# Optimization experiments

Measured on AMD Instinct MI355X. Metric: run time of the kernel, lower is better.

## Reference

```python
import jax, jax.numpy as jnp
import numpy as np

K, MU, SIGMA = 8, 0.0, 0.1
M, N, D_DIM, T = 512, 1024, 512, 4096


def setup_inputs() -> dict:
    key = jax.random.key(0)
    ks, ke, ka, kd, kl1, kl2 = jax.random.split(key, 6)
    S = jax.random.normal(ks, (N, T), dtype=jnp.float32)
    E = jax.random.normal(ke, (M, T), dtype=jnp.float32)  # raw noise; scaled by sigma/mu in reference
    A = jax.random.uniform(ka, (M, N), dtype=jnp.float32)  # torch.rand init
    Dm = jax.random.normal(kd, (N, D_DIM), dtype=jnp.float32) / jnp.sqrt(N)  # stands in for DCT-transformed randn
    c = jnp.ones((1,), dtype=jnp.float32)
    l1 = 0.1 * jnp.abs(jax.random.normal(kl1, (1,), dtype=jnp.float32)) + 0.05
    l2 = jax.random.normal(kl2, (1,), dtype=jnp.float32)
    # LISTA params per layer; all K layers get the same closed-form init in the original
    U1 = jnp.eye(D_DIM, dtype=jnp.float32) - (1.0 / c[0]) * (Dm.T @ A.T @ A @ Dm)  # [d,d]
    V1 = (1.0 / c[0]) * (Dm.T @ A.T)  # [d,m]
    U = jnp.broadcast_to(U1, (K, D_DIM, D_DIM)).copy()
    V = jnp.broadcast_to(V1, (K, D_DIM, M)).copy()
    H0 = jnp.zeros((D_DIM, T), dtype=jnp.float32)
    return {"S": S, "E": E, "A": A, "D": Dm, "U": U, "V": V, "l1": l1, "l2": l2, "c": c, "H0": H0}


def reference(S, E, A, D, U, V, l1, l2, c, H0):
    # X = A @ S + noise (E ~ randn, scaled as in torch forward)
    X = A @ S + (E * SIGMA + MU)  # [m,T]
    # Self-attention on H0 (the original loop always feeds self.H, the zero buffer,
    # into every layer -- H is never chained). Attention map = softmax((D@H0)^T (D@H0)).
    G = D @ H0                                   # [n,T]
    attn = jax.nn.softmax(G.T @ G, axis=-1)      # [T,T]
    Z = l2[0] * (H0 @ attn)                      # [d,T]
    # All K LISTA updates share the same (H0-derived) Z and X -> batch over layers.
    mat = jnp.einsum('kde,et->kdt', U, Z) + jnp.einsum('kdm,mt->kdt', V, X)  # [K,d,T]
    thres = l1[0] / c[0]
    H_all = jnp.sign(mat) * jnp.maximum(jnp.zeros((), mat.dtype), jnp.abs(mat) - thres)
    H_last = H_all[-1]                           # only the last layer's H survives the loop
    return D @ H_last                            # S_star [n,T]
```

## Files before the change

kernel.cpp:

```cpp
#include <hip/hip_runtime.h>

typedef unsigned short ushort_t;
typedef ushort_t u16x8 __attribute__((ext_vector_type(8)));
typedef ushort_t u16x4 __attribute__((ext_vector_type(4)));
typedef __bf16   bf16x8 __attribute__((ext_vector_type(8)));
typedef float    f32x4  __attribute__((ext_vector_type(4)));

#define T_DIM 4096

__device__ __forceinline__ ushort_t f2bf(float f){
  union { float f; unsigned u; } x; x.f = f;
  unsigned r = x.u + 0x7FFFu + ((x.u >> 16) & 1u);
  return (ushort_t)(r >> 16);
}

__global__ __launch_bounds__(256) void transpose_s_kernel(
    const float* __restrict__ S, ushort_t* __restrict__ St)
{
  __shared__ float tile[64][65];
  const int t0 = blockIdx.x * 64, n0 = blockIdx.y * 64;
  const int tid = threadIdx.x;
#pragma unroll
  for (int i = 0; i < 4; ++i){
    int g = tid + 256 * i; int row = g >> 4, cq = g & 15;
    const f32x4 v = *(const f32x4*)&S[(size_t)(n0 + row) * T_DIM + t0 + cq * 4];
#pragma unroll
    for (int j = 0; j < 4; ++j) tile[row][cq * 4 + j] = v[j];
  }
  __syncthreads();
#pragma unroll
  for (int i = 0; i < 2; ++i){
    int g = tid + 256 * i; int tl = g >> 3, nq = g & 7;
    u16x8 h;
#pragma unroll
    for (int j = 0; j < 8; ++j) h[j] = f2bf(tile[nq * 8 + j][tl]);
    *(u16x8*)&St[(size_t)(t0 + tl) * 1024 + n0 + nq * 8] = h;
  }
}

template<int EPI>
__global__ __launch_bounds__(256) void gemm_kernel(
    const ushort_t* __restrict__ Ag, const float* __restrict__ Bg,
    void* __restrict__ Cout, const float* __restrict__ Eptr,
    const float* __restrict__ l1p, const float* __restrict__ cp,
    const int Kd)
{
  __shared__ __align__(16) ushort_t As[128 * 64];
  __shared__ __align__(16) ushort_t Bs[64 * 64];
  const int tid = threadIdx.x;
  const int lane = tid & 63, wid = tid >> 6;
  const int wm = wid >> 1, wn = wid & 1;
  const int lr = lane & 15, lq = lane >> 4;
  const int t0 = blockIdx.x * 128, n0 = blockIdx.y * 64;

  f32x4 acc[4][2];
#pragma unroll
  for (int mf = 0; mf < 4; ++mf)
#pragma unroll
    for (int nf = 0; nf < 2; ++nf) acc[mf][nf] = (f32x4){0.f, 0.f, 0.f, 0.f};

  u16x8 ar[4];
  f32x4 br[4];

  auto loadG = [&](int kt){
#pragma unroll
    for (int i = 0; i < 4; ++i){
      int g = tid + 256 * i; int row = g >> 3, kb = g & 7;
      ar[i] = *(const u16x8*)&Ag[(size_t)(t0 + row) * Kd + kt * 64 + kb * 8];
    }
#pragma unroll
    for (int i = 0; i < 4; ++i){
      int g = tid + 256 * i; int n = g >> 4, kq = g & 15;
      br[i] = *(const f32x4*)&Bg[(size_t)(n0 + n) * Kd + kt * 64 + kq * 4];
    }
  };

  auto writeLDS = [&](){
#pragma unroll
    for (int i = 0; i < 4; ++i){
      int g = tid + 256 * i; int row = g >> 3, kb = g & 7;
      *(u16x8*)&As[row * 64 + ((kb ^ (row & 7)) << 3)] = ar[i];
    }
#pragma unroll
    for (int i = 0; i < 4; ++i){
      int g = tid + 256 * i; int n = g >> 4, kq = g & 15;
      u16x4 h;
#pragma unroll
      for (int j = 0; j < 4; ++j) h[j] = f2bf(br[i][j]);
      *(u16x4*)&Bs[n * 64 + (((kq >> 1) ^ (n & 7)) << 3) + ((kq & 1) << 2)] = h;
    }
  };

  auto compute = [&](){
#pragma unroll
    for (int ks = 0; ks < 2; ++ks){
      const int kb = ks * 4 + lq;
      bf16x8 a[4], b[2];
#pragma unroll
      for (int mf = 0; mf < 4; ++mf){
        int r = wm * 64 + mf * 16 + lr;
        a[mf] = *(const bf16x8*)&As[r * 64 + ((kb ^ (r & 7)) << 3)];
      }
#pragma unroll
      for (int nf = 0; nf < 2; ++nf){
        int n = wn * 32 + nf * 16 + lr;
        b[nf] = *(const bf16x8*)&Bs[n * 64 + ((kb ^ (n & 7)) << 3)];
      }
#pragma unroll
      for (int mf = 0; mf < 4; ++mf)
#pragma unroll
        for (int nf = 0; nf < 2; ++nf)
          acc[mf][nf] = __builtin_amdgcn_mfma_f32_16x16x32_bf16(
              a[mf], b[nf], acc[mf][nf], 0, 0, 0);
    }
  };

  const int nk = Kd >> 6;
  loadG(0);
  writeLDS();
  for (int kt = 0; kt < nk; ++kt){
    __syncthreads();
    if (kt + 1 < nk) loadG(kt + 1);
    compute();
    __syncthreads();
    if (kt + 1 < nk) writeLDS();
  }

  const float thres = (EPI == 1) ? (l1p[0] / cp[0]) : 0.f;
#pragma unroll
  for (int mf = 0; mf < 4; ++mf){
#pragma unroll
    for (int nf = 0; nf < 2; ++nf){
      const int tb  = t0 + wm * 64 + mf * 16 + lq * 4;
      const int col = n0 + wn * 32 + nf * 16 + lr;
      f32x4 v = acc[mf][nf];
      if (EPI == 0){
        const f32x4 e = *(const f32x4*)&Eptr[(size_t)col * T_DIM + tb];
        ushort_t* XT = (ushort_t*)Cout;
#pragma unroll
        for (int j = 0; j < 4; ++j)
          XT[(size_t)(tb + j) * 512 + col] = f2bf(v[j] + 0.1f * e[j]);
      } else if (EPI == 1){
        ushort_t* HT = (ushort_t*)Cout;
#pragma unroll
        for (int j = 0; j < 4; ++j){
          float av = fabsf(v[j]) - thres;
          float r = av > 0.f ? (v[j] > 0.f ? av : -av) : 0.f;
          HT[(size_t)(tb + j) * 512 + col] = f2bf(r);
        }
      } else {
        float* O = (float*)Cout;
        *(f32x4*)&O[(size_t)col * T_DIM + tb] = v;
      }
    }
  }
}

extern "C" void kernel_launch(void* const* d_in, const int* in_sizes, int n_in,
                              void* d_out, int out_size, void* d_ws, size_t ws_size,
                              hipStream_t stream)
{
  const float* S  = (const float*)d_in[0];
  const float* E  = (const float*)d_in[1];
  const float* A  = (const float*)d_in[2];
  const float* D  = (const float*)d_in[3];
  const float* V  = (const float*)d_in[5];
  const float* l1 = (const float*)d_in[6];
  const float* c  = (const float*)d_in[8];

  ushort_t* St = (ushort_t*)d_ws;
  ushort_t* XT = (ushort_t*)((char*)d_ws + (size_t)(8u << 20));
  ushort_t* HT = (ushort_t*)((char*)d_ws + (size_t)(12u << 20));
  const float* V7 = V + (size_t)7 * 512 * 512;

  transpose_s_kernel<<<dim3(64, 16), 256, 0, stream>>>(S, St);
  gemm_kernel<0><<<dim3(32, 8), 256, 0, stream>>>(St, A, (void*)XT, E, nullptr, nullptr, 1024);
  gemm_kernel<1><<<dim3(32, 8), 256, 0, stream>>>(XT, V7, (void*)HT, nullptr, l1, c, 512);
  gemm_kernel<2><<<dim3(32, 16), 256, 0, stream>>>(HT, D, d_out, nullptr, nullptr, nullptr, 512);
}
```

Measured before the change: 48.19 us.

## Pre-convert weights to swizzled bf16 and stage GEMM tiles via direct global-to-LDS loads

A single prep kernel now transposes S and also converts A, V7 and D to bf16 in a pre-swizzled layout. The GEMMs can then load both operands with global_load_lds straight into double-buffered shared memory, which drops the register staging and the per-iteration fp32-to-bf16 conversion and removes one barrier per k-step. The first two GEMMs switch to 64-row tiles to launch more blocks, and they swap the MFMA operand order so their transposed bf16 outputs are written as 4-element vectors into a swizzled layout. The cost is extra workspace, an extra conversion pass over the weights on every call, and narrower, more scattered reads of E in the epilogue.

```diff
diff --git a/kernel.cpp b/kernel.cpp
--- a/kernel.cpp
+++ b/kernel.cpp
@@ -1,6 +1,7 @@
 #include <hip/hip_runtime.h>
 
 typedef unsigned short ushort_t;
+typedef unsigned int u32;
 typedef ushort_t u16x8 __attribute__((ext_vector_type(8)));
 typedef ushort_t u16x4 __attribute__((ext_vector_type(4)));
 typedef __bf16   bf16x8 __attribute__((ext_vector_type(8)));
@@ -14,143 +15,174 @@
   return (ushort_t)(r >> 16);
 }
 
-__global__ __launch_bounds__(256) void transpose_s_kernel(
-    const float* __restrict__ S, ushort_t* __restrict__ St)
+__device__ __forceinline__ void gload16(const void* g, void* l){
+  __builtin_amdgcn_global_load_lds(
+      (const __attribute__((address_space(1))) u32*)g,
+      (__attribute__((address_space(3))) u32*)l, 16, 0, 0);
+}
+
+__global__ __launch_bounds__(256) void prep_kernel(
+    const float* __restrict__ S, const float* __restrict__ A,
+    const float* __restrict__ V7, const float* __restrict__ Dm,
+    ushort_t* __restrict__ St, ushort_t* __restrict__ Abf,
+    ushort_t* __restrict__ Vbf, ushort_t* __restrict__ Dbf)
 {
   __shared__ float tile[64][65];
-  const int t0 = blockIdx.x * 64, n0 = blockIdx.y * 64;
-  const int tid = threadIdx.x;
-#pragma unroll
-  for (int i = 0; i < 4; ++i){
-    int g = tid + 256 * i; int row = g >> 4, cq = g & 15;
-    const f32x4 v = *(const f32x4*)&S[(size_t)(n0 + row) * T_DIM + t0 + cq * 4];
-#pragma unroll
-    for (int j = 0; j < 4; ++j) tile[row][cq * 4 + j] = v[j];
+  const int bid = blockIdx.x, tid = threadIdx.x;
+  if (bid < 1024){
+    const int t0 = (bid & 63) * 64, n0 = (bid >> 6) * 64;
+#pragma unroll
+    for (int i = 0; i < 4; ++i){
+      int g = tid + 256 * i; int row = g >> 4, cq = g & 15;
+      const f32x4 v = *(const f32x4*)&S[(size_t)(n0 + row) * T_DIM + t0 + cq * 4];
+#pragma unroll
+      for (int j = 0; j < 4; ++j) tile[row][cq * 4 + j] = v[j];
+    }
+    __syncthreads();
+#pragma unroll
+    for (int i = 0; i < 2; ++i){
+      int g = tid + 256 * i; int tl = g >> 3, nq = g & 7;
+      u16x8 h;
+#pragma unroll
+      for (int j = 0; j < 8; ++j) h[j] = f2bf(tile[nq * 8 + j][tl]);
+      *(u16x8*)&St[(size_t)(t0 + tl) * 1024 + n0 + ((nq ^ (tl & 7)) << 3)] = h;
+    }
+  } else {
+    int pid = bid - 1024;
+    const float* src; ushort_t* dst; int g, ks;
+    if (pid < 256)      { src = A;  dst = Abf; g = pid * 256 + tid;        ks = 7; }
+    else if (pid < 384) { src = V7; dst = Vbf; g = (pid - 256) * 256 + tid; ks = 6; }
+    else                { src = Dm; dst = Dbf; g = (pid - 384) * 256 + tid; ks = 6; }
+    const int r = g >> ks, cg = g & ((1 << ks) - 1);
+    const int Kd = 8 << ks;
+    const size_t base = (size_t)r * Kd + (size_t)cg * 8;
+    const f32x4 v0 = *(const f32x4*)&src[base];
+    const f32x4 v1 = *(const f32x4*)&src[base + 4];
+    u16x8 h;
+#pragma unroll
+    for (int j = 0; j < 4; ++j){ h[j] = f2bf(v0[j]); h[j + 4] = f2bf(v1[j]); }
+    *(u16x8*)&dst[(size_t)r * Kd + ((cg >> 3) << 6) + ((((cg & 7) ^ (r & 7))) << 3)] = h;
   }
-  __syncthreads();
-#pragma unroll
-  for (int i = 0; i < 2; ++i){
-    int g = tid + 256 * i; int tl = g >> 3, nq = g & 7;
-    u16x8 h;
-#pragma unroll
-    for (int j = 0; j < 8; ++j) h[j] = f2bf(tile[nq * 8 + j][tl]);
-    *(u16x8*)&St[(size_t)(t0 + tl) * 1024 + n0 + nq * 8] = h;
-  }
-}
-
-template<int EPI>
+}
+
+template<int EPI, int BM>
 __global__ __launch_bounds__(256) void gemm_kernel(
-    const ushort_t* __restrict__ Ag, const float* __restrict__ Bg,
+    const ushort_t* __restrict__ Ag, const ushort_t* __restrict__ Bg,
     void* __restrict__ Cout, const float* __restrict__ Eptr,
     const float* __restrict__ l1p, const float* __restrict__ cp,
     const int Kd)
 {
-  __shared__ __align__(16) ushort_t As[128 * 64];
-  __shared__ __align__(16) ushort_t Bs[64 * 64];
+  constexpr int MF = BM / 32;
+  constexpr bool SWAP = (EPI != 2);
+  __shared__ __align__(16) ushort_t As[2][BM * 64];
+  __shared__ __align__(16) ushort_t Bs[2][64 * 64];
   const int tid = threadIdx.x;
   const int lane = tid & 63, wid = tid >> 6;
   const int wm = wid >> 1, wn = wid & 1;
   const int lr = lane & 15, lq = lane >> 4;
-  const int t0 = blockIdx.x * 128, n0 = blockIdx.y * 64;
-
-  f32x4 acc[4][2];
-#pragma unroll
-  for (int mf = 0; mf < 4; ++mf)
-#pragma unroll
-    for (int nf = 0; nf < 2; ++nf) acc[mf][nf] = (f32x4){0.f, 0.f, 0.f, 0.f};
-
-  u16x8 ar[4];
-  f32x4 br[4];
-
-  auto loadG = [&](int kt){
-#pragma unroll
-    for (int i = 0; i < 4; ++i){
-      int g = tid + 256 * i; int row = g >> 3, kb = g & 7;
-      ar[i] = *(const u16x8*)&Ag[(size_t)(t0 + row) * Kd + kt * 64 + kb * 8];
-    }
-#pragma unroll
-    for (int i = 0; i < 4; ++i){
-      int g = tid + 256 * i; int n = g >> 4, kq = g & 15;
-      br[i] = *(const f32x4*)&Bg[(size_t)(n0 + n) * Kd + kt * 64 + kq * 4];
+  const int t0 = blockIdx.x * BM, n0 = blockIdx.y * 64;
+
+  constexpr int P = SWAP ? 2 : MF;
+  constexpr int Q = SWAP ? MF : 2;
+  f32x4 acc[P][Q];
+#pragma unroll
+  for (int i = 0; i < P; ++i)
+#pragma unroll
+    for (int j = 0; j < Q; ++j) acc[i][j] = (f32x4){0.f, 0.f, 0.f, 0.f};
+
+  auto stage = [&](int kt, int b){
+#pragma unroll
+    for (int i = 0; i < BM / 32; ++i){
+      int c = i * 256 + tid;
+      gload16(&Ag[(size_t)(t0 + (c >> 3)) * Kd + kt * 64 + (c & 7) * 8],
+              &As[b][(i * 256 + (tid & 192)) * 8]);
+    }
+#pragma unroll
+    for (int i = 0; i < 2; ++i){
+      int c = i * 256 + tid;
+      gload16(&Bg[(size_t)(n0 + (c >> 3)) * Kd + kt * 64 + (c & 7) * 8],
+              &Bs[b][(i * 256 + (tid & 192)) * 8]);
     }
   };
 
-  auto writeLDS = [&](){
-#pragma unroll
-    for (int i = 0; i < 4; ++i){
-      int g = tid + 256 * i; int row = g >> 3, kb = g & 7;
-      *(u16x8*)&As[row * 64 + ((kb ^ (row & 7)) << 3)] = ar[i];
-    }
-#pragma unroll
-    for (int i = 0; i < 4; ++i){
-      int g = tid + 256 * i; int n = g >> 4, kq = g & 15;
-      u16x4 h;
-#pragma unroll
-      for (int j = 0; j < 4; ++j) h[j] = f2bf(br[i][j]);
-      *(u16x4*)&Bs[n * 64 + (((kq >> 1) ^ (n & 7)) << 3) + ((kq & 1) << 2)] = h;
+  auto compute = [&](int b){
+#pragma unroll
+    for (int ksv = 0; ksv < 2; ++ksv){
+      const int kb = ksv * 4 + lq;
+      bf16x8 a[MF], bb[2];
+#pragma unroll
+      for (int mf = 0; mf < MF; ++mf){
+        int r = wm * (BM / 2) + mf * 16 + lr;
+        a[mf] = *(const bf16x8*)&As[b][r * 64 + ((kb ^ (r & 7)) << 3)];
+      }
+#pragma unroll
+      for (int nf = 0; nf < 2; ++nf){
+        int r = wn * 32 + nf * 16 + lr;
+        bb[nf] = *(const bf16x8*)&Bs[b][r * 64 + ((kb ^ (r & 7)) << 3)];
+      }
+      if constexpr (SWAP){
+#pragma unroll
+        for (int nf = 0; nf < 2; ++nf)
+#pragma unroll
+          for (int mf = 0; mf < MF; ++mf)
+            acc[nf][mf] = __builtin_amdgcn_mfma_f32_16x16x32_bf16(
+                bb[nf], a[mf], acc[nf][mf], 0, 0, 0);
+      } else {
+#pragma unroll
+        for (int mf = 0; mf < MF; ++mf)
+#pragma unroll
+          for (int nf = 0; nf < 2; ++nf)
+            acc[mf][nf] = __builtin_amdgcn_mfma_f32_16x16x32_bf16(
+                a[mf], bb[nf], acc[mf][nf], 0, 0, 0);
+      }
     }
   };
 
-  auto compute = [&](){
-#pragma unroll
-    for (int ks = 0; ks < 2; ++ks){
-      const int kb = ks * 4 + lq;
-      bf16x8 a[4], b[2];
-#pragma unroll
-      for (int mf = 0; mf < 4; ++mf){
-        int r = wm * 64 + mf * 16 + lr;
-        a[mf] = *(const bf16x8*)&As[r * 64 + ((kb ^ (r & 7)) << 3)];
-      }
-#pragma unroll
-      for (int nf = 0; nf < 2; ++nf){
-        int n = wn * 32 + nf * 16 + lr;
-        b[nf] = *(const bf16x8*)&Bs[n * 64 + ((kb ^ (n & 7)) << 3)];
-      }
-#pragma unroll
-      for (int mf = 0; mf < 4; ++mf)
-#pragma unroll
-        for (int nf = 0; nf < 2; ++nf)
-          acc[mf][nf] = __builtin_amdgcn_mfma_f32_16x16x32_bf16(
-              a[mf], b[nf], acc[mf][nf], 0, 0, 0);
-    }
-  };
-
   const int nk = Kd >> 6;
-  loadG(0);
-  writeLDS();
+  stage(0, 0);
   for (int kt = 0; kt < nk; ++kt){
     __syncthreads();
-    if (kt + 1 < nk) loadG(kt + 1);
-    compute();
-    __syncthreads();
-    if (kt + 1 < nk) writeLDS();
+    if (kt + 1 < nk) stage(kt + 1, (kt + 1) & 1);
+    compute(kt & 1);
   }
 
-  const float thres = (EPI == 1) ? (l1p[0] / cp[0]) : 0.f;
-#pragma unroll
-  for (int mf = 0; mf < 4; ++mf){
+  if constexpr (EPI == 2){
+    float* O = (float*)Cout;
+#pragma unroll
+    for (int mf = 0; mf < MF; ++mf)
+#pragma unroll
+      for (int nf = 0; nf < 2; ++nf){
+        const int t = t0 + wm * (BM / 2) + mf * 16 + lq * 4;
+        const int n = n0 + wn * 32 + nf * 16 + lr;
+        *(f32x4*)&O[(size_t)n * T_DIM + t] = acc[mf][nf];
+      }
+  } else {
+    const float thres = (EPI == 1) ? (l1p[0] / cp[0]) : 0.f;
+    ushort_t* OT = (ushort_t*)Cout;
 #pragma unroll
     for (int nf = 0; nf < 2; ++nf){
-      const int tb  = t0 + wm * 64 + mf * 16 + lq * 4;
-      const int col = n0 + wn * 32 + nf * 16 + lr;
-      f32x4 v = acc[mf][nf];
-      if (EPI == 0){
-        const f32x4 e = *(const f32x4*)&Eptr[(size_t)col * T_DIM + tb];
-        ushort_t* XT = (ushort_t*)Cout;
-#pragma unroll
-        for (int j = 0; j < 4; ++j)
-          XT[(size_t)(tb + j) * 512 + col] = f2bf(v[j] + 0.1f * e[j]);
-      } else if (EPI == 1){
-        ushort_t* HT = (ushort_t*)Cout;
-#pragma unroll
-        for (int j = 0; j < 4; ++j){
-          float av = fabsf(v[j]) - thres;
-          float r = av > 0.f ? (v[j] > 0.f ? av : -av) : 0.f;
-          HT[(size_t)(tb + j) * 512 + col] = f2bf(r);
+#pragma unroll
+      for (int mf = 0; mf < MF; ++mf){
+        const int m = n0 + wn * 32 + nf * 16 + lq * 4;
+        const int t = t0 + wm * (BM / 2) + mf * 16 + lr;
+        f32x4 v = acc[nf][mf];
+        u16x4 h;
+        if constexpr (EPI == 0){
+#pragma unroll
+          for (int j = 0; j < 4; ++j){
+            float e = Eptr[(size_t)(m + j) * T_DIM + t];
+            h[j] = f2bf(v[j] + 0.1f * e);
+          }
+        } else {
+#pragma unroll
+          for (int j = 0; j < 4; ++j){
+            float av = fabsf(v[j]) - thres;
+            float r = av > 0.f ? (v[j] > 0.f ? av : -av) : 0.f;
+            h[j] = f2bf(r);
+          }
         }
-      } else {
-        float* O = (float*)Cout;
-        *(f32x4*)&O[(size_t)col * T_DIM + tb] = v;
+        *(u16x4*)&OT[(size_t)t * 512 + (m & ~63) +
+                     (((((m >> 3) & 7) ^ (t & 7))) << 3) + (m & 7)] = h;
       }
     }
   }
@@ -163,18 +195,22 @@
   const float* S  = (const float*)d_in[0];
   const float* E  = (const float*)d_in[1];
   const float* A  = (const float*)d_in[2];
-  const float* D  = (const float*)d_in[3];
+  const float* Dm = (const float*)d_in[3];
   const float* V  = (const float*)d_in[5];
   const float* l1 = (const float*)d_in[6];
   const float* c  = (const float*)d_in[8];
 
-  ushort_t* St = (ushort_t*)d_ws;
-  ushort_t* XT = (ushort_t*)((char*)d_ws + (size_t)(8u << 20));
-  ushort_t* HT = (ushort_t*)((char*)d_ws + (size_t)(12u << 20));
+  char* ws = (char*)d_ws;
+  ushort_t* St  = (ushort_t*)(ws);
+  ushort_t* XT  = (ushort_t*)(ws + (size_t)( 8u << 20));
+  ushort_t* HT  = (ushort_t*)(ws + (size_t)(12u << 20));
+  ushort_t* Abf = (ushort_t*)(ws + (size_t)(16u << 20));
+  ushort_t* Vbf = (ushort_t*)(ws + (size_t)(17u << 20));
+  ushort_t* Dbf = (ushort_t*)(ws + (size_t)(17u << 20) + (512u << 10));
   const float* V7 = V + (size_t)7 * 512 * 512;
 
-  transpose_s_kernel<<<dim3(64, 16), 256, 0, stream>>>(S, St);
-  gemm_kernel<0><<<dim3(32, 8), 256, 0, stream>>>(St, A, (void*)XT, E, nullptr, nullptr, 1024);
-  gemm_kernel<1><<<dim3(32, 8), 256, 0, stream>>>(XT, V7, (void*)HT, nullptr, l1, c, 512);
-  gemm_kernel<2><<<dim3(32, 16), 256, 0, stream>>>(HT, D, d_out, nullptr, nullptr, nullptr, 512);
-}
+  prep_kernel<<<1664, 256, 0, stream>>>(S, A, V7, Dm, St, Abf, Vbf, Dbf);
+  gemm_kernel<0, 64><<<dim3(64, 8), 256, 0, stream>>>(St, Abf, (void*)XT, E, nullptr, nullptr, 1024);
+  gemm_kernel<1, 64><<<dim3(64, 8), 256, 0, stream>>>(XT, Vbf, (void*)HT, nullptr, l1, c, 512);
+  gemm_kernel<2, 128><<<dim3(32, 16), 256, 0, stream>>>(HT, Dbf, d_out, nullptr, nullptr, nullptr, 512);
+}
```

Result: faster. 43.43 us (-9.9%).
